# Optimization experiments

Measured on AMD Instinct MI355X. Metric: run time of the kernel, lower is better.

The kernel has to match this reference:

```python
import jax, jax.numpy as jnp
import numpy as np

B, L, H, O = 2048, 256, 512, 1  # batch, input_len, hidden_size, output_size
EPS = 1e-5

def setup_inputs() -> dict:
    key = jax.random.key(0)
    ks = jax.random.split(key, 16)
    s = 0.05
    return {
        "x": jax.random.normal(ks[0], (B, 1, O), jnp.float32),
        "hidden": jax.random.normal(ks[1], (1, B, H), jnp.float32),
        "encoder_outputs": jax.random.normal(ks[2], (B, L, H), jnp.float32),
        # weights stored [in, out] (transposed torch Linear convention)
        "emb_W": jax.random.normal(ks[3], (O, H), jnp.float32) * s,
        "emb_b": jax.random.normal(ks[4], (H,), jnp.float32) * s,
        "attn_W": jax.random.normal(ks[5], (2 * H, L), jnp.float32) * s,
        "attn_b": jax.random.normal(ks[6], (L,), jnp.float32) * s,
        "comb_W": jax.random.normal(ks[7], (2 * H, H), jnp.float32) * s,
        "comb_b": jax.random.normal(ks[8], (H,), jnp.float32) * s,
        "gru_Wih": jax.random.normal(ks[9], (H, 3 * H), jnp.float32) * s,
        "gru_Whh": jax.random.normal(ks[10], (H, 3 * H), jnp.float32) * s,
        "gru_bih": jax.random.normal(ks[11], (3 * H,), jnp.float32) * s,
        "gru_bhh": jax.random.normal(ks[12], (3 * H,), jnp.float32) * s,
        "out_W": jax.random.normal(ks[13], (H, O), jnp.float32) * s,
        "out_b": jax.random.normal(ks[14], (O,), jnp.float32) * s,
    }

def reference(x, hidden, encoder_outputs, emb_W, emb_b, attn_W, attn_b,
              comb_W, comb_b, gru_Wih, gru_Whh, gru_bih, gru_bhh, out_W, out_b):
    # embedding + InstanceNorm1d over hidden dim (C=1 channel, length=H), no affine
    embedded = x @ emb_W + emb_b                      # [B,1,H]
    mu = jnp.mean(embedded, axis=-1, keepdims=True)
    var = jnp.var(embedded, axis=-1, keepdims=True)   # biased var, matches torch
    embedded = (embedded - mu) * jax.lax.rsqrt(var + EPS)
    # dropout = identity (inference)
    h_b = jnp.transpose(hidden, (1, 0, 2))            # [B,1,H]
    attn_logits = jnp.concatenate([embedded, h_b], axis=2) @ attn_W + attn_b  # [B,1,L]
    attn_weights = jax.nn.softmax(attn_logits, axis=2)
    attn_applied = jnp.einsum('bql,bld->bqd', attn_weights, encoder_outputs)  # [B,1,H]
    out = jnp.concatenate([embedded, attn_applied], axis=2) @ comb_W + comb_b
    out = jax.nn.relu(out)                            # [B,1,H]
    # single GRU step (num_layers=1, seq_len=1)
    xt = out[:, 0, :]                                 # [B,H]
    h0 = hidden[0]                                    # [B,H]
    gi = xt @ gru_Wih + gru_bih                       # [B,3H]
    gh = h0 @ gru_Whh + gru_bhh
    i_r, i_z, i_n = jnp.split(gi, 3, axis=-1)
    h_r, h_z, h_n = jnp.split(gh, 3, axis=-1)
    r = jax.nn.sigmoid(i_r + h_r)
    z = jax.nn.sigmoid(i_z + h_z)
    n = jnp.tanh(i_n + r * h_n)
    h_new = (1.0 - z) * n + z * h0                    # [B,H]
    output = h_new[:, None, :] @ out_W + out_b        # [B,1,O]
    return output, h_new[None, :, :], attn_weights
```

## Files before the change

### kernel.cpp

```cpp
#include <hip/hip_runtime.h>
#include <math.h>

#define NB 2048
#define NL 256
#define NH 512

typedef unsigned short ushort_t;
typedef unsigned int uint_t;
typedef short s16x8 __attribute__((ext_vector_type(8)));
typedef short s16x4 __attribute__((ext_vector_type(4)));
typedef float f32x4 __attribute__((ext_vector_type(4)));

__device__ __forceinline__ float wsum(float v){
  #pragma unroll
  for (int o = 32; o; o >>= 1) v += __shfl_xor(v, o);
  return v;
}
__device__ __forceinline__ float wmax(float v){
  #pragma unroll
  for (int o = 32; o; o >>= 1) v = fmaxf(v, __shfl_xor(v, o));
  return v;
}
__device__ __forceinline__ ushort_t f2bf(float f){
  union { float f; unsigned u; } v; v.f = f;
  unsigned r = v.u + 0x7fffu + ((v.u >> 16) & 1u);
  return (ushort_t)(r >> 16);
}

__global__ __launch_bounds__(256)
void kTiny(const float* __restrict__ eW, const float* __restrict__ eb,
           const float* __restrict__ attn_W, const float* __restrict__ comb_W,
           const float* __restrict__ out_b,
           ushort_t* __restrict__ WTA, float* __restrict__ stats,
           float* __restrict__ p, float* __restrict__ q,
           float* __restrict__ p2, float* __restrict__ q2,
           float* __restrict__ out0)
{
  const int bid = blockIdx.x, tid = threadIdx.x;
  if (bid < 32) {
    const int bx = bid & 3, by = bid >> 2;
    const int c = bx*64 + (tid & 63);
    const int ksub = by*64 + (tid >> 6)*16;
    ushort_t vals[16];
    #pragma unroll
    for (int kk = 0; kk < 16; ++kk)
      vals[kk] = f2bf(attn_W[(size_t)(512 + ksub + kk)*NL + c]);
    *(s16x8*)&WTA[(size_t)c*512 + ksub]     = *(s16x8*)&vals[0];
    *(s16x8*)&WTA[(size_t)c*512 + ksub + 8] = *(s16x8*)&vals[8];
    return;
  }
  if (bid > 44) {
    out0[(bid-45)*256 + tid] = out_b[0];
    return;
  }
  {
    __shared__ float rw[4], rb[4];
    __shared__ float pa[4][64], pb[4][64];
    const int lane = tid & 63, wv = tid >> 6;
    float swv = eW[tid] + eW[tid + 256];
    float sbv = eb[tid] + eb[tid + 256];
    swv = wsum(swv); sbv = wsum(sbv);
    if (lane == 0) { rw[wv] = swv; rb[wv] = sbv; }
    __syncthreads();
    const float mW = (rw[0]+rw[1]+rw[2]+rw[3]) * (1.f/NH);
    const float mb = (rb[0]+rb[1]+rb[2]+rb[3]) * (1.f/NH);

    if (bid == 44) {
      float u0 = eW[tid]-mW, u1 = eW[tid+256]-mW;
      float v0 = eb[tid]-mb, v1 = eb[tid+256]-mb;
      float s2 = u0*u0 + u1*u1, s3 = u0*v0 + u1*v1, s4 = v0*v0 + v1*v1;
      s2 = wsum(s2); s3 = wsum(s3); s4 = wsum(s4);
      if (lane == 0) { pa[0][wv] = s2; pa[1][wv] = s3; pa[2][wv] = s4; }
      __syncthreads();
      if (tid == 0) {
        stats[0] = mW; stats[1] = mb;
        stats[2] = pa[0][0]+pa[0][1]+pa[0][2]+pa[0][3];
        stats[3] = pa[1][0]+pa[1][1]+pa[1][2]+pa[1][3];
        stats[4] = pa[2][0]+pa[2][1]+pa[2][2]+pa[2][3];
      }
      return;
    }
    const int bid2 = bid - 32;
    const float* Wsrc; int ldw, c0; float *op, *oq;
    if (bid2 < 4) { Wsrc = attn_W; ldw = NL; c0 = bid2*64;     op = p  + c0; oq = q  + c0; }
    else          { Wsrc = comb_W; ldw = NH; c0 = (bid2-4)*64; op = p2 + c0; oq = q2 + c0; }
    const int c = c0 + lane;
    const int hc = tid >> 6;
    float ap = 0.f, aq = 0.f;
    #pragma unroll 4
    for (int h = hc*128; h < hc*128 + 128; ++h) {
      float w = Wsrc[(size_t)h*ldw + c];
      ap = fmaf(eW[h]-mW, w, ap);
      aq = fmaf(eb[h]-mb, w, aq);
    }
    pa[hc][lane] = ap; pb[hc][lane] = aq;
    __syncthreads();
    if (hc == 0) {
      op[lane] = pa[0][lane]+pa[1][lane]+pa[2][lane]+pa[3][lane];
      oq[lane] = pb[0][lane]+pb[1][lane]+pb[2][lane]+pb[3][lane];
    }
  }
}

__global__ __launch_bounds__(256)
void kLogits(const float* __restrict__ hidden, const ushort_t* __restrict__ WTA,
             const float* __restrict__ x, const float* __restrict__ stats,
             const float* __restrict__ p, const float* __restrict__ q,
             const float* __restrict__ attn_b, float* __restrict__ logits)
{
  __shared__ ushort_t As[128][72];
  __shared__ ushort_t Bs[64][72];
  const int tid = threadIdx.x, lane = tid & 63, wr = tid >> 6;
  const int m0 = blockIdx.x * 128, n0 = blockIdx.y * 64;

  f32x4 acc[2][4];
  #pragma unroll
  for (int i = 0; i < 2; ++i)
    #pragma unroll
    for (int j = 0; j < 4; ++j)
      acc[i][j] = (f32x4){0.f,0.f,0.f,0.f};

  const int srow = tid >> 3, scol = (tid & 7) * 8;
  for (int kt = 0; kt < 512; kt += 64) {
    __syncthreads();
    #pragma unroll
    for (int it = 0; it < 4; ++it) {
      const int r = srow + it*32;
      const float* hp = hidden + (size_t)(m0+r)*NH + kt + scol;
      float4 v0 = *(const float4*)hp;
      float4 v1 = *(const float4*)(hp + 4);
      s16x8 o;
      o[0]=f2bf(v0.x); o[1]=f2bf(v0.y); o[2]=f2bf(v0.z); o[3]=f2bf(v0.w);
      o[4]=f2bf(v1.x); o[5]=f2bf(v1.y); o[6]=f2bf(v1.z); o[7]=f2bf(v1.w);
      *(s16x8*)&As[r][scol] = o;
    }
    #pragma unroll
    for (int it = 0; it < 2; ++it) {
      const int r = srow + it*32;
      *(s16x8*)&Bs[r][scol] = *(const s16x8*)&WTA[(size_t)(n0+r)*512 + kt + scol];
    }
    __syncthreads();
    #pragma unroll
    for (int ks = 0; ks < 2; ++ks) {
      const int ko = ks*32 + (lane >> 4)*8;
      s16x8 af[2], bfr[4];
      #pragma unroll
      for (int i = 0; i < 2; ++i) af[i]  = *(const s16x8*)&As[wr*32 + i*16 + (lane & 15)][ko];
      #pragma unroll
      for (int j = 0; j < 4; ++j) bfr[j] = *(const s16x8*)&Bs[j*16 + (lane & 15)][ko];
      #pragma unroll
      for (int i = 0; i < 2; ++i)
        #pragma unroll
        for (int j = 0; j < 4; ++j)
          acc[i][j] = __builtin_amdgcn_mfma_f32_16x16x32_bf16(af[i], bfr[j], acc[i][j], 0, 0, 0);
    }
  }

  const float S2 = stats[2], S3 = stats[3], S4 = stats[4];
  #pragma unroll
  for (int i = 0; i < 2; ++i) {
    #pragma unroll
    for (int reg = 0; reg < 4; ++reg) {
      const int row = m0 + wr*32 + i*16 + ((lane >> 4) << 2) + reg;
      const float xv = x[row];
      const float rs = rsqrtf((xv*xv*S2 + 2.f*xv*S3 + S4)*(1.0f/NH) + 1e-5f);
      const float al = xv*rs, be = rs;
      #pragma unroll
      for (int j = 0; j < 4; ++j) {
        const int col = n0 + j*16 + (lane & 15);
        logits[(size_t)row*NL + col] = acc[i][j][reg] + attn_b[col] + al*p[col] + be*q[col];
      }
    }
  }
}

__global__ __launch_bounds__(256)
void kStreamMega(const float* __restrict__ hidden,
                 const float* __restrict__ Wih, const float* __restrict__ Whh,
                 const float* __restrict__ comb_W,
                 const float* __restrict__ logits, const float* __restrict__ enc,
                 ushort_t* __restrict__ A2, ushort_t* __restrict__ WTG,
                 ushort_t* __restrict__ WTC,
                 float* __restrict__ attn_out, ushort_t* __restrict__ ABF)
{
  const int bid = blockIdx.x, tid = threadIdx.x;
  if (bid < 2048) {
    __shared__ float wl[NL];
    __shared__ __align__(16) float4 ps[128];
    __shared__ float sred[4];
    const int lane = tid & 63, wv = tid >> 6;
    const int b = bid;

    float lg = logits[(size_t)b*NL + tid];
    float m = wmax(lg);
    if (lane == 0) sred[wv] = m;
    __syncthreads();
    m = fmaxf(fmaxf(sred[0], sred[1]), fmaxf(sred[2], sred[3]));
    float e = expf(lg - m);
    float s = wsum(e);
    __syncthreads();
    if (lane == 0) sred[wv] = s;
    __syncthreads();
    const float inv = 1.f / (sred[0] + sred[1] + sred[2] + sred[3]);
    e *= inv;
    wl[tid] = e;
    attn_out[(size_t)b*NL + tid] = e;
    __syncthreads();

    const int col = tid & 127, half = tid >> 7;
    const f32x4* ep = (const f32x4*)(enc + (size_t)b*NL*NH);
    float4 acc = {0.f,0.f,0.f,0.f};
    #pragma unroll 4
    for (int l = half*128; l < half*128 + 128; ++l) {
      float w = wl[l];
      f32x4 ev = __builtin_nontemporal_load(ep + l*(NH/4) + col);
      acc.x = fmaf(w,ev[0],acc.x); acc.y = fmaf(w,ev[1],acc.y);
      acc.z = fmaf(w,ev[2],acc.z); acc.w = fmaf(w,ev[3],acc.w);
    }
    if (half == 0) ps[col] = acc;
    __syncthreads();
    if (half == 1) {
      float4 o = ps[col];
      o.x += acc.x; o.y += acc.y; o.z += acc.z; o.w += acc.w;
      s16x4 ov; ov[0]=f2bf(o.x); ov[1]=f2bf(o.y); ov[2]=f2bf(o.z); ov[3]=f2bf(o.w);
      *(s16x4*)&ABF[(size_t)b*NH + col*4] = ov;
    }
    return;
  }
  if (bid < 2560) {
    const int idx = ((bid-2048)*256 + tid) * 8;
    const int b = idx >> 9, h = idx & 511;
    float4 v0 = *(const float4*)(hidden + idx);
    float4 v1 = *(const float4*)(hidden + idx + 4);
    s16x8 o;
    o[0]=f2bf(v0.x); o[1]=f2bf(v0.y); o[2]=f2bf(v0.z); o[3]=f2bf(v0.w);
    o[4]=f2bf(v1.x); o[5]=f2bf(v1.y); o[6]=f2bf(v1.z); o[7]=f2bf(v1.w);
    *(s16x8*)&A2[(size_t)b*1024 + 512 + h] = o;
    return;
  }
  if (bid < 3072) {
    const int b2 = bid - 2560, bx = b2 & 31, by = b2 >> 5;
    const int n = bx*64 + (tid & 63);
    const int ksub = by*64 + (tid >> 6)*16;
    const int g = n >> 6, t = (n >> 4) & 3, c = (g << 4) | (n & 15);
    const int sc = (t == 0) ? c : (t == 1) ? (512 + c) : (1024 + c);
    ushort_t vals[16];
    #pragma unroll
    for (int kk = 0; kk < 16; ++kk) {
      int k = ksub + kk;
      float v;
      if (k < 512) v = (t == 3) ? 0.f : Wih[(size_t)k*1536 + sc];
      else         v = (t == 2) ? 0.f : Whh[(size_t)(k-512)*1536 + sc];
      vals[kk] = f2bf(v);
    }
    *(s16x8*)&WTG[(size_t)n*1024 + ksub]     = *(s16x8*)&vals[0];
    *(s16x8*)&WTG[(size_t)n*1024 + ksub + 8] = *(s16x8*)&vals[8];
    return;
  }
  {
    const int b2 = bid - 3072, bx = b2 & 7, by = b2 >> 3;
    const int c = bx*64 + (tid & 63);
    const int ksub = by*64 + (tid >> 6)*16;
    ushort_t vals[16];
    #pragma unroll
    for (int kk = 0; kk < 16; ++kk)
      vals[kk] = f2bf(comb_W[(size_t)(512 + ksub + kk)*NH + c]);
    *(s16x8*)&WTC[(size_t)c*512 + ksub]     = *(s16x8*)&vals[0];
    *(s16x8*)&WTC[(size_t)c*512 + ksub + 8] = *(s16x8*)&vals[8];
  }
}

__global__ __launch_bounds__(256)
void kComb(const ushort_t* __restrict__ ABF, const ushort_t* __restrict__ WTC,
           const float* __restrict__ x, const float* __restrict__ stats,
           const float* __restrict__ p2, const float* __restrict__ q2,
           const float* __restrict__ comb_b, ushort_t* __restrict__ A2)
{
  __shared__ ushort_t As[128][72];
  __shared__ ushort_t Bs[64][72];
  const int tid = threadIdx.x, lane = tid & 63, wr = tid >> 6;
  const int m0 = blockIdx.x * 128, n0 = blockIdx.y * 64;

  f32x4 acc[2][4];
  #pragma unroll
  for (int i = 0; i < 2; ++i)
    #pragma unroll
    for (int j = 0; j < 4; ++j)
      acc[i][j] = (f32x4){0.f,0.f,0.f,0.f};

  const int srow = tid >> 3, scol = (tid & 7) * 8;
  for (int kt = 0; kt < 512; kt += 64) {
    __syncthreads();
    #pragma unroll
    for (int it = 0; it < 4; ++it) {
      const int r = srow + it*32;
      *(s16x8*)&As[r][scol] = *(const s16x8*)&ABF[(size_t)(m0+r)*512 + kt + scol];
    }
    #pragma unroll
    for (int it = 0; it < 2; ++it) {
      const int r = srow + it*32;
      *(s16x8*)&Bs[r][scol] = *(const s16x8*)&WTC[(size_t)(n0+r)*512 + kt + scol];
    }
    __syncthreads();
    #pragma unroll
    for (int ks = 0; ks < 2; ++ks) {
      const int ko = ks*32 + (lane >> 4)*8;
      s16x8 af[2], bfr[4];
      #pragma unroll
      for (int i = 0; i < 2; ++i) af[i]  = *(const s16x8*)&As[wr*32 + i*16 + (lane & 15)][ko];
      #pragma unroll
      for (int j = 0; j < 4; ++j) bfr[j] = *(const s16x8*)&Bs[j*16 + (lane & 15)][ko];
      #pragma unroll
      for (int i = 0; i < 2; ++i)
        #pragma unroll
        for (int j = 0; j < 4; ++j)
          acc[i][j] = __builtin_amdgcn_mfma_f32_16x16x32_bf16(af[i], bfr[j], acc[i][j], 0, 0, 0);
    }
  }

  const float S2 = stats[2], S3 = stats[3], S4 = stats[4];
  #pragma unroll
  for (int i = 0; i < 2; ++i) {
    #pragma unroll
    for (int reg = 0; reg < 4; ++reg) {
      const int row = m0 + wr*32 + i*16 + ((lane >> 4) << 2) + reg;
      const float xv = x[row];
      const float rs = rsqrtf((xv*xv*S2 + 2.f*xv*S3 + S4)*(1.0f/NH) + 1e-5f);
      const float al = xv*rs, be = rs;
      #pragma unroll
      for (int j = 0; j < 4; ++j) {
        const int col = n0 + j*16 + (lane & 15);
        float v = acc[i][j][reg] + comb_b[col] + al*p2[col] + be*q2[col];
        A2[(size_t)row*1024 + col] = f2bf(fmaxf(v, 0.f));
      }
    }
  }
}

__global__ __launch_bounds__(256)
void kGRU(const ushort_t* __restrict__ A, const ushort_t* __restrict__ Bt,
          const float* __restrict__ bih, const float* __restrict__ bhh,
          const float* __restrict__ hidden, const float* __restrict__ out_W,
          float* __restrict__ h_out, float* __restrict__ out0)
{
  __shared__ ushort_t As[128][72];
  __shared__ ushort_t Bs[64][72];
  const int tid = threadIdx.x, lane = tid & 63, wr = tid >> 6;
  const int m0 = blockIdx.x * 128, n0 = blockIdx.y * 64;
  const int K = 1024;

  f32x4 acc[2][4];
  #pragma unroll
  for (int i = 0; i < 2; ++i)
    #pragma unroll
    for (int j = 0; j < 4; ++j)
      acc[i][j] = (f32x4){0.f,0.f,0.f,0.f};

  const int srow = tid >> 3, scol = (tid & 7) * 8;
  for (int kt = 0; kt < K; kt += 64) {
    __syncthreads();
    #pragma unroll
    for (int it = 0; it < 4; ++it) {
      const int r = srow + it*32;
      *(s16x8*)&As[r][scol] = *(const s16x8*)&A[(size_t)(m0+r)*1024 + kt + scol];
    }
    #pragma unroll
    for (int it = 0; it < 2; ++it) {
      const int r = srow + it*32;
      *(s16x8*)&Bs[r][scol] = *(const s16x8*)&Bt[(size_t)(n0+r)*K + kt + scol];
    }
    __syncthreads();
    #pragma unroll
    for (int ks = 0; ks < 2; ++ks) {
      const int ko = ks*32 + (lane >> 4)*8;
      s16x8 af[2], bfr[4];
      #pragma unroll
      for (int i = 0; i < 2; ++i) af[i]  = *(const s16x8*)&As[wr*32 + i*16 + (lane & 15)][ko];
      #pragma unroll
      for (int j = 0; j < 4; ++j) bfr[j] = *(const s16x8*)&Bs[j*16 + (lane & 15)][ko];
      #pragma unroll
      for (int i = 0; i < 2; ++i)
        #pragma unroll
        for (int j = 0; j < 4; ++j)
          acc[i][j] = __builtin_amdgcn_mfma_f32_16x16x32_bf16(af[i], bfr[j], acc[i][j], 0, 0, 0);
    }
  }

  const int g = n0 >> 6;
  const int hcol = (g << 4) | (lane & 15);
  const float b_r = bih[hcol]        + bhh[hcol];
  const float b_z = bih[512 + hcol]  + bhh[512 + hcol];
  const float b_i = bih[1024 + hcol];
  const float b_h = bhh[1024 + hcol];
  const float ow  = out_W[hcol];
  #pragma unroll
  for (int i = 0; i < 2; ++i) {
    #pragma unroll
    for (int reg = 0; reg < 4; ++reg) {
      const int row = m0 + wr*32 + i*16 + ((lane >> 4) << 2) + reg;
      float rv = 1.f / (1.f + expf(-(acc[i][0][reg] + b_r)));
      float zv = 1.f / (1.f + expf(-(acc[i][1][reg] + b_z)));
      float nv = tanhf(acc[i][2][reg] + b_i + rv * (acc[i][3][reg] + b_h));
      float h0v = hidden[(size_t)row*NH + hcol];
      float hn = nv + zv * (h0v - nv);
      h_out[(size_t)row*NH + hcol] = hn;
      float partial = hn * ow;
      #pragma unroll
      for (int o = 1; o < 16; o <<= 1) partial += __shfl_xor(partial, o);
      if ((lane & 15) == 0) atomicAdd(&out0[row], partial);
    }
  }
}

extern "C" void kernel_launch(void* const* d_in, const int* in_sizes, int n_in,
                              void* d_out, int out_size, void* d_ws, size_t ws_size,
                              hipStream_t stream)
{
  const float* x      = (const float*)d_in[0];
  const float* hidden = (const float*)d_in[1];
  const float* enc    = (const float*)d_in[2];
  const float* emb_W  = (const float*)d_in[3];
  const float* emb_b  = (const float*)d_in[4];
  const float* attn_W = (const float*)d_in[5];
  const float* attn_b = (const float*)d_in[6];
  const float* comb_W = (const float*)d_in[7];
  const float* comb_b = (const float*)d_in[8];
  const float* Wih    = (const float*)d_in[9];
  const float* Whh    = (const float*)d_in[10];
  const float* bih    = (const float*)d_in[11];
  const float* bhh    = (const float*)d_in[12];
  const float* out_W  = (const float*)d_in[13];
  const float* out_b  = (const float*)d_in[14];

  float* out      = (float*)d_out;
  float* out0     = out;
  float* out_h    = out + NB;
  float* out_attn = out + NB + (size_t)NB*NH;

  float* wsf    = (float*)d_ws;
  float* stats  = wsf;
  float* p      = wsf + 16;
  float* q      = wsf + 272;
  float* p2     = wsf + 528;
  float* q2     = wsf + 1040;
  float* logits = wsf + 2048;
  ushort_t* usb = (ushort_t*)(wsf + 526400);
  ushort_t* A2  = usb;
  ushort_t* ABF = usb + 2097152;
  ushort_t* WTA = usb + 3145728;
  ushort_t* WTC = usb + 3276800;
  ushort_t* WTG = usb + 3538944;

  kTiny<<<53, 256, 0, stream>>>(emb_W, emb_b, attn_W, comb_W, out_b,
                                WTA, stats, p, q, p2, q2, out0);
  kLogits<<<dim3(16, 4), 256, 0, stream>>>(hidden, WTA, x, stats, p, q,
                                           attn_b, logits);
  kStreamMega<<<3136, 256, 0, stream>>>(hidden, Wih, Whh, comb_W, logits, enc,
                                        A2, WTG, WTC, out_attn, ABF);
  kComb<<<dim3(16, 8), 256, 0, stream>>>(ABF, WTC, x, stats, p2, q2, comb_b, A2);
  kGRU<<<dim3(16, 32), 256, 0, stream>>>(A2, WTG, bih, bhh, hidden, out_W,
                                         out_h, out0);
}
```

Before: 262.3 us.

## Skip zero-padded GRU weight blocks and move comb projections into stream kernel

The GRU GEMM now splits K into the input half and the hidden half. In each half it loads and multiplies only the three gate tiles that are nonzero, skipping the structurally zero blocks of the packed weight matrix. The comb_W projection blocks and the out0 initialisation move from the tiny prologue kernel into the large streaming kernel, so the serial first kernel has fewer blocks. The GRU change trims MFMA work and B-tile loads by about a quarter, at the cost of code duplication.

```diff
diff --git a/kernel.cpp b/kernel.cpp
--- a/kernel.cpp
+++ b/kernel.cpp
@@ -29,12 +29,9 @@
 
 __global__ __launch_bounds__(256)
 void kTiny(const float* __restrict__ eW, const float* __restrict__ eb,
-           const float* __restrict__ attn_W, const float* __restrict__ comb_W,
-           const float* __restrict__ out_b,
+           const float* __restrict__ attn_W,
            ushort_t* __restrict__ WTA, float* __restrict__ stats,
-           float* __restrict__ p, float* __restrict__ q,
-           float* __restrict__ p2, float* __restrict__ q2,
-           float* __restrict__ out0)
+           float* __restrict__ p, float* __restrict__ q)
 {
   const int bid = blockIdx.x, tid = threadIdx.x;
   if (bid < 32) {
@@ -47,10 +44,6 @@
       vals[kk] = f2bf(attn_W[(size_t)(512 + ksub + kk)*NL + c]);
     *(s16x8*)&WTA[(size_t)c*512 + ksub]     = *(s16x8*)&vals[0];
     *(s16x8*)&WTA[(size_t)c*512 + ksub + 8] = *(s16x8*)&vals[8];
-    return;
-  }
-  if (bid > 44) {
-    out0[(bid-45)*256 + tid] = out_b[0];
     return;
   }
   {
@@ -65,7 +58,7 @@
     const float mW = (rw[0]+rw[1]+rw[2]+rw[3]) * (1.f/NH);
     const float mb = (rb[0]+rb[1]+rb[2]+rb[3]) * (1.f/NH);
 
-    if (bid == 44) {
+    if (bid == 36) {
       float u0 = eW[tid]-mW, u1 = eW[tid+256]-mW;
       float v0 = eb[tid]-mb, v1 = eb[tid+256]-mb;
       float s2 = u0*u0 + u1*u1, s3 = u0*v0 + u1*v1, s4 = v0*v0 + v1*v1;
@@ -80,24 +73,20 @@
       }
       return;
     }
-    const int bid2 = bid - 32;
-    const float* Wsrc; int ldw, c0; float *op, *oq;
-    if (bid2 < 4) { Wsrc = attn_W; ldw = NL; c0 = bid2*64;     op = p  + c0; oq = q  + c0; }
-    else          { Wsrc = comb_W; ldw = NH; c0 = (bid2-4)*64; op = p2 + c0; oq = q2 + c0; }
-    const int c = c0 + lane;
+    const int c = (bid - 32)*64 + lane;
     const int hc = tid >> 6;
     float ap = 0.f, aq = 0.f;
     #pragma unroll 4
     for (int h = hc*128; h < hc*128 + 128; ++h) {
-      float w = Wsrc[(size_t)h*ldw + c];
+      float w = attn_W[(size_t)h*NL + c];
       ap = fmaf(eW[h]-mW, w, ap);
       aq = fmaf(eb[h]-mb, w, aq);
     }
     pa[hc][lane] = ap; pb[hc][lane] = aq;
     __syncthreads();
     if (hc == 0) {
-      op[lane] = pa[0][lane]+pa[1][lane]+pa[2][lane]+pa[3][lane];
-      oq[lane] = pb[0][lane]+pb[1][lane]+pb[2][lane]+pb[3][lane];
+      p[c] = pa[0][lane]+pa[1][lane]+pa[2][lane]+pa[3][lane];
+      q[c] = pb[0][lane]+pb[1][lane]+pb[2][lane]+pb[3][lane];
     }
   }
 }
@@ -178,9 +167,13 @@
 void kStreamMega(const float* __restrict__ hidden,
                  const float* __restrict__ Wih, const float* __restrict__ Whh,
                  const float* __restrict__ comb_W,
+                 const float* __restrict__ eW, const float* __restrict__ eb,
+                 const float* __restrict__ out_b,
                  const float* __restrict__ logits, const float* __restrict__ enc,
                  ushort_t* __restrict__ A2, ushort_t* __restrict__ WTG,
                  ushort_t* __restrict__ WTC,
+                 float* __restrict__ p2, float* __restrict__ q2,
+                 float* __restrict__ out0,
                  float* __restrict__ attn_out, ushort_t* __restrict__ ABF)
 {
   const int bid = blockIdx.x, tid = threadIdx.x;
@@ -257,7 +250,7 @@
     *(s16x8*)&WTG[(size_t)n*1024 + ksub + 8] = *(s16x8*)&vals[8];
     return;
   }
-  {
+  if (bid < 3136) {
     const int b2 = bid - 3072, bx = b2 & 7, by = b2 >> 3;
     const int c = bx*64 + (tid & 63);
     const int ksub = by*64 + (tid >> 6)*16;
@@ -267,7 +260,37 @@
       vals[kk] = f2bf(comb_W[(size_t)(512 + ksub + kk)*NH + c]);
     *(s16x8*)&WTC[(size_t)c*512 + ksub]     = *(s16x8*)&vals[0];
     *(s16x8*)&WTC[(size_t)c*512 + ksub + 8] = *(s16x8*)&vals[8];
-  }
+    return;
+  }
+  if (bid < 3144) {
+    __shared__ float rw[4], rb[4];
+    __shared__ float pa[4][64], pb[4][64];
+    const int lane = tid & 63, wv = tid >> 6;
+    float swv = eW[tid] + eW[tid + 256];
+    float sbv = eb[tid] + eb[tid + 256];
+    swv = wsum(swv); sbv = wsum(sbv);
+    if (lane == 0) { rw[wv] = swv; rb[wv] = sbv; }
+    __syncthreads();
+    const float mW = (rw[0]+rw[1]+rw[2]+rw[3]) * (1.f/NH);
+    const float mb = (rb[0]+rb[1]+rb[2]+rb[3]) * (1.f/NH);
+    const int c = (bid - 3136)*64 + lane;
+    const int hc = tid >> 6;
+    float ap = 0.f, aq = 0.f;
+    #pragma unroll 4
+    for (int h = hc*128; h < hc*128 + 128; ++h) {
+      float w = comb_W[(size_t)h*NH + c];
+      ap = fmaf(eW[h]-mW, w, ap);
+      aq = fmaf(eb[h]-mb, w, aq);
+    }
+    pa[hc][lane] = ap; pb[hc][lane] = aq;
+    __syncthreads();
+    if (hc == 0) {
+      p2[c] = pa[0][lane]+pa[1][lane]+pa[2][lane]+pa[3][lane];
+      q2[c] = pb[0][lane]+pb[1][lane]+pb[2][lane]+pb[3][lane];
+    }
+    return;
+  }
+  out0[(bid-3144)*256 + tid] = out_b[0];
 }
 
 __global__ __launch_bounds__(256)
@@ -347,7 +370,6 @@
   __shared__ ushort_t Bs[64][72];
   const int tid = threadIdx.x, lane = tid & 63, wr = tid >> 6;
   const int m0 = blockIdx.x * 128, n0 = blockIdx.y * 64;
-  const int K = 1024;
 
   f32x4 acc[2][4];
   #pragma unroll
@@ -357,32 +379,69 @@
       acc[i][j] = (f32x4){0.f,0.f,0.f,0.f};
 
   const int srow = tid >> 3, scol = (tid & 7) * 8;
-  for (int kt = 0; kt < K; kt += 64) {
+
+  for (int kt = 0; kt < 512; kt += 64) {
     __syncthreads();
     #pragma unroll
     for (int it = 0; it < 4; ++it) {
       const int r = srow + it*32;
       *(s16x8*)&As[r][scol] = *(const s16x8*)&A[(size_t)(m0+r)*1024 + kt + scol];
     }
-    #pragma unroll
-    for (int it = 0; it < 2; ++it) {
-      const int r = srow + it*32;
-      *(s16x8*)&Bs[r][scol] = *(const s16x8*)&Bt[(size_t)(n0+r)*K + kt + scol];
+    {
+      *(s16x8*)&Bs[srow][scol] = *(const s16x8*)&Bt[(size_t)(n0+srow)*1024 + kt + scol];
+      if (srow < 16) {
+        const int r = srow + 32;
+        *(s16x8*)&Bs[r][scol] = *(const s16x8*)&Bt[(size_t)(n0+r)*1024 + kt + scol];
+      }
     }
     __syncthreads();
     #pragma unroll
     for (int ks = 0; ks < 2; ++ks) {
       const int ko = ks*32 + (lane >> 4)*8;
-      s16x8 af[2], bfr[4];
-      #pragma unroll
-      for (int i = 0; i < 2; ++i) af[i]  = *(const s16x8*)&As[wr*32 + i*16 + (lane & 15)][ko];
-      #pragma unroll
-      for (int j = 0; j < 4; ++j) bfr[j] = *(const s16x8*)&Bs[j*16 + (lane & 15)][ko];
-      #pragma unroll
-      for (int i = 0; i < 2; ++i)
-        #pragma unroll
-        for (int j = 0; j < 4; ++j)
-          acc[i][j] = __builtin_amdgcn_mfma_f32_16x16x32_bf16(af[i], bfr[j], acc[i][j], 0, 0, 0);
+      s16x8 af[2], b0, b1, b2;
+      #pragma unroll
+      for (int i = 0; i < 2; ++i) af[i] = *(const s16x8*)&As[wr*32 + i*16 + (lane & 15)][ko];
+      b0 = *(const s16x8*)&Bs[0*16 + (lane & 15)][ko];
+      b1 = *(const s16x8*)&Bs[1*16 + (lane & 15)][ko];
+      b2 = *(const s16x8*)&Bs[2*16 + (lane & 15)][ko];
+      #pragma unroll
+      for (int i = 0; i < 2; ++i) {
+        acc[i][0] = __builtin_amdgcn_mfma_f32_16x16x32_bf16(af[i], b0, acc[i][0], 0, 0, 0);
+        acc[i][1] = __builtin_amdgcn_mfma_f32_16x16x32_bf16(af[i], b1, acc[i][1], 0, 0, 0);
+        acc[i][2] = __builtin_amdgcn_mfma_f32_16x16x32_bf16(af[i], b2, acc[i][2], 0, 0, 0);
+      }
+    }
+  }
+  for (int kt = 512; kt < 1024; kt += 64) {
+    __syncthreads();
+    #pragma unroll
+    for (int it = 0; it < 4; ++it) {
+      const int r = srow + it*32;
+      *(s16x8*)&As[r][scol] = *(const s16x8*)&A[(size_t)(m0+r)*1024 + kt + scol];
+    }
+    {
+      *(s16x8*)&Bs[srow][scol] = *(const s16x8*)&Bt[(size_t)(n0+srow)*1024 + kt + scol];
+      if (srow >= 16) {
+        const int r = srow + 32;
+        *(s16x8*)&Bs[r][scol] = *(const s16x8*)&Bt[(size_t)(n0+r)*1024 + kt + scol];
+      }
+    }
+    __syncthreads();
+    #pragma unroll
+    for (int ks = 0; ks < 2; ++ks) {
+      const int ko = ks*32 + (lane >> 4)*8;
+      s16x8 af[2], b0, b1, b3;
+      #pragma unroll
+      for (int i = 0; i < 2; ++i) af[i] = *(const s16x8*)&As[wr*32 + i*16 + (lane & 15)][ko];
+      b0 = *(const s16x8*)&Bs[0*16 + (lane & 15)][ko];
+      b1 = *(const s16x8*)&Bs[1*16 + (lane & 15)][ko];
+      b3 = *(const s16x8*)&Bs[3*16 + (lane & 15)][ko];
+      #pragma unroll
+      for (int i = 0; i < 2; ++i) {
+        acc[i][0] = __builtin_amdgcn_mfma_f32_16x16x32_bf16(af[i], b0, acc[i][0], 0, 0, 0);
+        acc[i][1] = __builtin_amdgcn_mfma_f32_16x16x32_bf16(af[i], b1, acc[i][1], 0, 0, 0);
+        acc[i][3] = __builtin_amdgcn_mfma_f32_16x16x32_bf16(af[i], b3, acc[i][3], 0, 0, 0);
+      }
     }
   }
 
@@ -451,12 +510,12 @@
   ushort_t* WTC = usb + 3276800;
   ushort_t* WTG = usb + 3538944;
 
-  kTiny<<<53, 256, 0, stream>>>(emb_W, emb_b, attn_W, comb_W, out_b,
-                                WTA, stats, p, q, p2, q2, out0);
+  kTiny<<<37, 256, 0, stream>>>(emb_W, emb_b, attn_W, WTA, stats, p, q);
   kLogits<<<dim3(16, 4), 256, 0, stream>>>(hidden, WTA, x, stats, p, q,
                                            attn_b, logits);
-  kStreamMega<<<3136, 256, 0, stream>>>(hidden, Wih, Whh, comb_W, logits, enc,
-                                        A2, WTG, WTC, out_attn, ABF);
+  kStreamMega<<<3152, 256, 0, stream>>>(hidden, Wih, Whh, comb_W, emb_W, emb_b,
+                                        out_b, logits, enc, A2, WTG, WTC,
+                                        p2, q2, out0, out_attn, ABF);
   kComb<<<dim3(16, 8), 256, 0, stream>>>(ABF, WTC, x, stats, p2, q2, comb_b, A2);
   kGRU<<<dim3(16, 32), 256, 0, stream>>>(A2, WTG, bih, bhh, hidden, out_W,
                                          out_h, out0);
```

New measurement: 246.2 us, median of 2. 6.1% less time.
